# Kernel optimization log

Hardware: AMD Instinct MI355X
Metric: run time of the kernel (lower is better)

Reference implementation:

```python
import jax, jax.numpy as jnp
import numpy as np

N_NODES = 100_000
N_EDGES = 1_600_000
N_GRAPHS = 512
D_NODE = 128
H = 128
L_EXTRA = 2  # model_layer - 1


def _bn(x, g, b, eps=1e-5):
    # BatchNorm1d, training-mode math (biased batch variance), eval dropout = identity
    mu = jnp.mean(x, axis=0)
    var = jnp.var(x, axis=0)
    return g * (x - mu) * jax.lax.rsqrt(var + eps) + b


def _gin_conv(x, src, dst, W1, b1, bng, bnb, W2, b2):
    # GINConv (eps=0): mlp(x + sum_{j->i} x_j); mlp = Lin -> BN -> ReLU -> Lin
    agg = jax.ops.segment_sum(x[src], dst, num_segments=x.shape[0])
    h = x + agg
    h = jax.nn.relu(_bn(h @ W1 + b1, bng, bnb))
    return h @ W2 + b2


def setup_inputs():
    key = jax.random.key(0)
    ks = jax.random.split(key, 24)
    s = 0.05
    d = {}
    d["x"] = jax.random.normal(ks[0], (N_NODES, D_NODE), dtype=jnp.float32)
    d["edge_index"] = jax.random.randint(ks[1], (2, N_EDGES), 0, N_NODES, dtype=jnp.int32)
    d["batch"] = jnp.sort(jax.random.randint(ks[2], (N_NODES,), 0, N_GRAPHS, dtype=jnp.int32))
    d["vn_emb"] = jax.random.normal(ks[3], (1, H)) * s
    # conv1 MLP: Linear(D_NODE, 2H) -> BN -> ReLU -> Linear(2H, H)
    d["c1_W1"] = jax.random.normal(ks[4], (D_NODE, 2 * H)) * s
    d["c1_b1"] = jnp.zeros((2 * H,))
    d["c1_bng"] = jnp.ones((2 * H,))
    d["c1_bnb"] = jnp.zeros((2 * H,))
    d["c1_W2"] = jax.random.normal(ks[5], (2 * H, H)) * s
    d["c1_b2"] = jnp.zeros((H,))
    d["bn1_g"] = jnp.ones((H,))
    d["bn1_b"] = jnp.zeros((H,))
    # stacked extra GIN layers (model_layer - 1)
    d["cW1"] = jax.random.normal(ks[6], (L_EXTRA, H, 2 * H)) * s
    d["cb1"] = jnp.zeros((L_EXTRA, 2 * H))
    d["cbng"] = jnp.ones((L_EXTRA, 2 * H))
    d["cbnb"] = jnp.zeros((L_EXTRA, 2 * H))
    d["cW2"] = jax.random.normal(ks[7], (L_EXTRA, 2 * H, H)) * s
    d["cb2"] = jnp.zeros((L_EXTRA, H))
    d["bns_g"] = jnp.ones((L_EXTRA, H))
    d["bns_b"] = jnp.zeros((L_EXTRA, H))
    # virtual node MLP: Lin(H,2H)->BN->ReLU->Lin(2H,H)->BN->ReLU->Dropout
    d["vW1"] = jax.random.normal(ks[8], (H, 2 * H)) * s
    d["vb1"] = jnp.zeros((2 * H,))
    d["vbn1_g"] = jnp.ones((2 * H,))
    d["vbn1_b"] = jnp.zeros((2 * H,))
    d["vW2"] = jax.random.normal(ks[9], (2 * H, H)) * s
    d["vb2"] = jnp.zeros((H,))
    d["vbn2_g"] = jnp.ones((H,))
    d["vbn2_b"] = jnp.zeros((H,))
    return d


def reference(x, edge_index, batch, vn_emb, c1_W1, c1_b1, c1_bng, c1_bnb, c1_W2, c1_b2,
              bn1_g, bn1_b, cW1, cb1, cbng, cbnb, cW2, cb2, bns_g, bns_b,
              vW1, vb1, vbn1_g, vbn1_b, vW2, vb2, vbn2_g, vbn2_b):
    src, dst = edge_index[0], edge_index[1]
    # virtual node feature per graph: Embedding(1, H) indexed with zeros
    vfeat = jnp.broadcast_to(vn_emb[0], (N_GRAPHS, H))
    # layer 1: dropout is identity in eval mode
    post = jax.nn.relu(_bn(_gin_conv(x, src, dst, c1_W1, c1_b1, c1_bng, c1_bnb, c1_W2, c1_b2), bn1_g, bn1_b))
    for i in range(L_EXTRA):
        post = post + vfeat[batch]                       # virtual-node broadcast
        post = _bn(_gin_conv(post, src, dst, cW1[i], cb1[i], cbng[i], cbnb[i], cW2[i], cb2[i]), bns_g[i], bns_b[i])
        if i < L_EXTRA - 1:
            post = jax.nn.relu(post)
            pooled = jax.ops.segment_sum(post, batch, num_segments=N_GRAPHS)  # GlobalAddPool
            z = pooled + vfeat
            z = jax.nn.relu(_bn(z @ vW1 + vb1, vbn1_g, vbn1_b))
            vfeat = jax.nn.relu(_bn(z @ vW2 + vb2, vbn2_g, vbn2_b))
    # readout: global mean pool over nodes per graph
    counts = jax.ops.segment_sum(jnp.ones((x.shape[0],), post.dtype), batch, num_segments=N_GRAPHS)
    out = jax.ops.segment_sum(post, batch, num_segments=N_GRAPHS) / jnp.maximum(counts, 1.0)[:, None]
    return out
```

## Files before the change

kernel.cpp:

```cpp
#include <hip/hip_runtime.h>

#define NN 100000
#define NE 1600000
#define NG 512
#define DH 128
#define DH2 256
#define SCB 98
#define NSTRIPE 32

typedef __attribute__((ext_vector_type(8))) _Float16 h8;
typedef __attribute__((ext_vector_type(2))) _Float16 h2;
typedef __attribute__((ext_vector_type(4))) float f4;

static inline size_t align256(size_t x) { return (x + 255) & ~size_t(255); }

__global__ __launch_bounds__(256) void countslot_k(const int* __restrict__ ei,
                                                   int* __restrict__ cursor,
                                                   int* __restrict__ slot) {
    int i = blockIdx.x * blockDim.x + threadIdx.x;
    int stride = gridDim.x * blockDim.x;
    for (int e = i; e < NE; e += stride)
        slot[e] = atomicAdd(&cursor[ei[NE + e]], 1);
}

__global__ __launch_bounds__(256) void place_k(const int* __restrict__ ei,
                                               const int* __restrict__ rowptr,
                                               const int* __restrict__ slot,
                                               int* __restrict__ esrc) {
    int i = blockIdx.x * blockDim.x + threadIdx.x;
    int stride = gridDim.x * blockDim.x;
    for (int e = i; e < NE; e += stride)
        esrc[rowptr[ei[NE + e]] + slot[e]] = ei[e];
}

__global__ __launch_bounds__(256) void scan1_k(const int* __restrict__ deg,
                                               int* __restrict__ part) {
    int i0 = blockIdx.x * 1024 + threadIdx.x * 4;
    int s = 0;
    if (i0 < NN) {
        int4 v = *(const int4*)(deg + i0);
        s = v.x + v.y + v.z + v.w;
    }
#pragma unroll
    for (int o = 1; o < 64; o <<= 1) s += __shfl_xor(s, o);
    __shared__ int ws[4];
    if ((threadIdx.x & 63) == 0) ws[threadIdx.x >> 6] = s;
    __syncthreads();
    if (threadIdx.x == 0) part[blockIdx.x] = ws[0] + ws[1] + ws[2] + ws[3];
}

__global__ void scan2_k(int* __restrict__ part, int* __restrict__ rowptr,
                        const int* __restrict__ batch, int* __restrict__ gcnt) {
    int t = threadIdx.x;
    __shared__ int wtot[2];
    int v = 0, s = 0;
    if (t < 128) {
        v = (t < SCB) ? part[t] : 0;
        s = v;
#pragma unroll
        for (int o = 1; o < 64; o <<= 1) {
            int u = __shfl_up(s, o);
            if ((t & 63) >= o) s += u;
        }
        if ((t & 63) == 63) wtot[t >> 6] = s;
    }
    __syncthreads();
    if (t < 128) {
        if (t >= 64) s += wtot[0];
        if (t < SCB) part[t] = s - v;
        if (t == SCB - 1) rowptr[NN] = s;
    }
    for (int g = t; g < NG; g += 256) {
        int lo = 0, hi = NN;
        while (lo < hi) { int m = (lo + hi) >> 1; if (batch[m] < g) lo = m + 1; else hi = m; }
        int b0 = lo;
        lo = 0; hi = NN;
        int g1 = g + 1;
        while (lo < hi) { int m = (lo + hi) >> 1; if (batch[m] < g1) lo = m + 1; else hi = m; }
        gcnt[g] = lo - b0;
    }
}

__global__ __launch_bounds__(256) void scan3_k(const int* __restrict__ deg,
                                               const int* __restrict__ part,
                                               int* __restrict__ rowptr) {
    int t = threadIdx.x;
    int i0 = blockIdx.x * 1024 + t * 4;
    int4 v = {0, 0, 0, 0};
    if (i0 < NN) v = *(const int4*)(deg + i0);
    int s = v.x + v.y + v.z + v.w;
    __shared__ int sc[256];
    sc[t] = s;
    __syncthreads();
    for (int o = 1; o < 256; o <<= 1) {
        int add = (t >= o) ? sc[t - o] : 0;
        __syncthreads();
        sc[t] += add;
        __syncthreads();
    }
    int excl = (t ? sc[t - 1] : 0) + part[blockIdx.x];
    if (i0 < NN) {
        int4 r;
        r.x = excl;
        r.y = excl + v.x;
        r.z = excl + v.x + v.y;
        r.w = excl + v.x + v.y + v.z;
        *(int4*)(rowptr + i0) = r;
    }
}

__global__ void castx_k(const float* __restrict__ x, _Float16* __restrict__ xh,
                        const float* __restrict__ emb, _Float16* __restrict__ vfeat) {
    int i = blockIdx.x * blockDim.x + threadIdx.x;
    if (i < NG * 16) {
        const float* e = emb + (i & 15) * 8;
        h8 v = {(_Float16)e[0], (_Float16)e[1], (_Float16)e[2], (_Float16)e[3],
                (_Float16)e[4], (_Float16)e[5], (_Float16)e[6], (_Float16)e[7]};
        ((h8*)vfeat)[i] = v;
    }
    if (i >= NN * 16) return;
    const float4* s = (const float4*)x + i * 2;
    float4 p = s[0], q = s[1];
    h8 h = {(_Float16)p.x, (_Float16)p.y, (_Float16)p.z, (_Float16)p.w,
            (_Float16)q.x, (_Float16)q.y, (_Float16)q.z, (_Float16)q.w};
    ((h8*)xh)[i] = h;
}

__global__ void zin_k(const float* __restrict__ pooled, const _Float16* __restrict__ vf,
                      _Float16* __restrict__ zb) {
    int i = blockIdx.x * blockDim.x + threadIdx.x;
    if (i < NG * DH) zb[i] = (_Float16)(pooled[i] + (float)vf[i]);
}

__global__ void addvn_k(_Float16* __restrict__ x, const _Float16* __restrict__ vfeat,
                        const int* __restrict__ batch) {
    int i = blockIdx.x * blockDim.x + threadIdx.x;
    if (i >= NN * 16) return;
    int row = i >> 4;
    int bg = batch[row];
    h8 u = ((h8*)x)[i];
    h8 v = ((const h8*)vfeat)[bg * 16 + (i & 15)];
    h8 o;
#pragma unroll
    for (int e = 0; e < 8; e++) o[e] = (_Float16)((float)u[e] + (float)v[e]);
    ((h8*)x)[i] = o;
}

__global__ void finalout_k(const float* __restrict__ pooled2, const int* __restrict__ gcnt,
                           float* __restrict__ outp) {
    int i = blockIdx.x * blockDim.x + threadIdx.x;
    if (i >= NG * DH) return;
    float cnt = (float)gcnt[i >> 7];
    outp[i] = pooled2[i] / fmaxf(cnt, 1.0f);
}

struct WPack {
    const float* w[8];
    _Float16* wt[8];
    int K[8];
    int N[8];
};
__global__ void wtrans_k(WPack p) {
    int id = blockIdx.z;
    const float* W = p.w[id];
    _Float16* Wt = p.wt[id];
    int K = p.K[id], N = p.N[id];
    int n0 = blockIdx.x * 32, k0 = blockIdx.y * 32;
    if (n0 >= N || k0 >= K) return;
    __shared__ float t[32][33];
    int tx = threadIdx.x & 31, ty = threadIdx.x >> 5;
    for (int i = 0; i < 32; i += 8)
        t[ty + i][tx] = W[(size_t)(k0 + ty + i) * N + n0 + tx];
    __syncthreads();
    for (int i = 0; i < 32; i += 8)
        Wt[(size_t)(n0 + ty + i) * K + k0 + tx] = (_Float16)t[tx][ty + i];
}

__global__ __launch_bounds__(256) void agg_k(const _Float16* __restrict__ xin,
                                             const int* __restrict__ rowptr,
                                             const int* __restrict__ esrc,
                                             _Float16* __restrict__ out) {
    int wave = threadIdx.x >> 6, lane = threadIdx.x & 63;
    int node = blockIdx.x * 4 + wave;
    if (node >= NN) return;
    const h2* xr = (const h2*)xin;
    h2 self = xr[(size_t)node * 64 + lane];
    float a0 = (float)self.x, a1 = (float)self.y;
    int beg = rowptr[node], end = rowptr[node + 1];
    int j = beg;
    for (; j + 7 < end; j += 8) {
        int s0 = esrc[j],     s1 = esrc[j + 1], s2 = esrc[j + 2], s3 = esrc[j + 3];
        int s4 = esrc[j + 4], s5 = esrc[j + 5], s6 = esrc[j + 6], s7 = esrc[j + 7];
        h2 u0 = xr[(size_t)s0 * 64 + lane];
        h2 u1 = xr[(size_t)s1 * 64 + lane];
        h2 u2 = xr[(size_t)s2 * 64 + lane];
        h2 u3 = xr[(size_t)s3 * 64 + lane];
        h2 u4 = xr[(size_t)s4 * 64 + lane];
        h2 u5 = xr[(size_t)s5 * 64 + lane];
        h2 u6 = xr[(size_t)s6 * 64 + lane];
        h2 u7 = xr[(size_t)s7 * 64 + lane];
        a0 += ((float)u0.x + (float)u1.x) + ((float)u2.x + (float)u3.x)
            + ((float)u4.x + (float)u5.x) + ((float)u6.x + (float)u7.x);
        a1 += ((float)u0.y + (float)u1.y) + ((float)u2.y + (float)u3.y)
            + ((float)u4.y + (float)u5.y) + ((float)u6.y + (float)u7.y);
    }
    for (; j < end; j++) {
        h2 u = xr[(size_t)esrc[j] * 64 + lane];
        a0 += (float)u.x; a1 += (float)u.y;
    }
    h2 o; o.x = (_Float16)a0; o.y = (_Float16)a1;
    ((h2*)out)[(size_t)node * 64 + lane] = o;
}

__global__ __launch_bounds__(256, 3) void gemmS_k(
        const _Float16* __restrict__ A, const _Float16* __restrict__ Wt,
        const float* __restrict__ bias,
        float* __restrict__ csum, float* __restrict__ csq, int M) {
    constexpr int K = 128;
    constexpr int LDA = K + 8;
    __shared__ __align__(16) _Float16 As[64 * LDA];
    __shared__ __align__(16) _Float16 Ws[128 * LDA];
    const int tid = threadIdx.x;
    const int lane = tid & 63;
    const int wave = tid >> 6;
    const int wr = wave >> 1;
    const int wc = wave & 1;
    const int lm = lane & 15, lq = lane >> 4;
    const int mB = blockIdx.x * 64;

    const int sr = tid >> 4;
    const int sc = (tid & 15) * 8;
#pragma unroll
    for (int rr = 0; rr < 64; rr += 16) {
        int gr = mB + rr + sr; if (gr >= M) gr = M - 1;
        *(h8*)&As[(rr + sr) * LDA + sc] = *(const h8*)&A[(size_t)gr * K + sc];
    }
#pragma unroll
    for (int rr = 0; rr < 128; rr += 16)
        *(h8*)&Ws[(rr + sr) * LDA + sc] = *(const h8*)&Wt[(size_t)(rr + sr) * K + sc];
    __syncthreads();

    f4 acc[2][8];
#pragma unroll
    for (int i = 0; i < 2; i++)
#pragma unroll
        for (int jj = 0; jj < 8; jj++) acc[i][jj] = (f4){0.f, 0.f, 0.f, 0.f};
#pragma unroll
    for (int ct = 0; ct < 2; ct++) {
        if (ct) {
            __syncthreads();
#pragma unroll
            for (int rr = 0; rr < 128; rr += 16)
                *(h8*)&Ws[(rr + sr) * LDA + sc] =
                    *(const h8*)&Wt[(size_t)(128 + rr + sr) * K + sc];
            __syncthreads();
        }
#pragma unroll
        for (int ks = 0; ks < 4; ks++) {
            h8 af[2], bf[4];
#pragma unroll
            for (int i = 0; i < 2; i++)
                af[i] = *(const h8*)&As[(wr * 32 + i * 16 + lm) * LDA + ks * 32 + lq * 8];
#pragma unroll
            for (int j = 0; j < 4; j++)
                bf[j] = *(const h8*)&Ws[(wc * 64 + j * 16 + lm) * LDA + ks * 32 + lq * 8];
#pragma unroll
            for (int i = 0; i < 2; i++)
#pragma unroll
                for (int j = 0; j < 4; j++)
                    acc[i][ct * 4 + j] =
                        __builtin_amdgcn_mfma_f32_16x16x32_f16(af[i], bf[j], acc[i][ct * 4 + j], 0, 0, 0);
        }
    }

    float bv[8];
#pragma unroll
    for (int jj = 0; jj < 8; jj++) bv[jj] = bias[(jj >> 2) * 128 + wc * 64 + (jj & 3) * 16 + lm];
    float ls[8] = {0, 0, 0, 0, 0, 0, 0, 0}, lsq[8] = {0, 0, 0, 0, 0, 0, 0, 0};
#pragma unroll
    for (int i = 0; i < 2; i++) {
        int row = wr * 32 + i * 16 + lq * 4;
#pragma unroll
        for (int jj = 0; jj < 8; jj++) {
#pragma unroll
            for (int r = 0; r < 4; r++) {
                if (mB + row + r < M) {
                    float v = acc[i][jj][r] + bv[jj];
                    ls[jj] += v; lsq[jj] += v * v;
                }
            }
        }
    }
    const int stripe = blockIdx.x & (NSTRIPE - 1);
#pragma unroll
    for (int jj = 0; jj < 8; jj++) {
        float s = ls[jj], q = lsq[jj];
        s += __shfl_xor(s, 16); s += __shfl_xor(s, 32);
        q += __shfl_xor(q, 16); q += __shfl_xor(q, 32);
        if (lq == 0) {
            int col = (jj >> 2) * 128 + wc * 64 + (jj & 3) * 16 + lm;
            atomicAdd(&csum[stripe * 256 + col], s);
            atomicAdd(&csq[stripe * 256 + col], q);
        }
    }
}

__global__ __launch_bounds__(256, 2) void gemmF_k(
        const _Float16* __restrict__ A,
        const _Float16* __restrict__ Wt1,
        const _Float16* __restrict__ Wt2,
        const float* __restrict__ b1v,
        const float* __restrict__ b2v,
        _Float16* __restrict__ C,
        float* __restrict__ csum, float* __restrict__ csq, int M,
        const float* __restrict__ csumIn, const float* __restrict__ csqIn,
        const float* __restrict__ g, const float* __restrict__ b) {
    constexpr int LDA = 136, LDH = 264;
    __shared__ __align__(16) _Float16 Hx[64 * LDH];
    __shared__ __align__(16) _Float16 Ws[128 * LDA];
    __shared__ float s_sc[256], s_sh[256];
    const int tid = threadIdx.x;
    const int lane = tid & 63;
    const int wave = tid >> 6;
    const int wr = wave >> 1;
    const int wc = wave & 1;
    const int lm = lane & 15, lq = lane >> 4;
    const int mB = blockIdx.x * 64;

    {
        float s = 0.f, q = 0.f;
        for (int st = 0; st < NSTRIPE; st++) {
            s += csumIn[st * 256 + tid];
            q += csqIn[st * 256 + tid];
        }
        float invM = 1.0f / (float)M;
        float mean = s * invM;
        float var = q * invM - mean * mean;
        float scv = g[tid] * rsqrtf(var + 1e-5f);
        s_sc[tid] = scv;
        s_sh[tid] = b[tid] - mean * scv;
    }

    const int sr = tid >> 4;
    const int sc = (tid & 15) * 8;
#pragma unroll
    for (int rr = 0; rr < 64; rr += 16) {
        int gr = mB + rr + sr; if (gr >= M) gr = M - 1;
        *(h8*)&Hx[(rr + sr) * LDA + sc] = *(const h8*)&A[(size_t)gr * 128 + sc];
    }
#pragma unroll
    for (int rr = 0; rr < 128; rr += 16)
        *(h8*)&Ws[(rr + sr) * LDA + sc] = *(const h8*)&Wt1[(size_t)(rr + sr) * 128 + sc];
    __syncthreads();

    f4 acc[2][8];
#pragma unroll
    for (int i = 0; i < 2; i++)
#pragma unroll
        for (int jj = 0; jj < 8; jj++) acc[i][jj] = (f4){0.f, 0.f, 0.f, 0.f};
#pragma unroll
    for (int ct = 0; ct < 2; ct++) {
        if (ct) {
            __syncthreads();
#pragma unroll
            for (int rr = 0; rr < 128; rr += 16)
                *(h8*)&Ws[(rr + sr) * LDA + sc] =
                    *(const h8*)&Wt1[(size_t)(128 + rr + sr) * 128 + sc];
            __syncthreads();
        }
#pragma unroll
        for (int ks = 0; ks < 4; ks++) {
            h8 af[2], bf[4];
#pragma unroll
            for (int i = 0; i < 2; i++)
                af[i] = *(const h8*)&Hx[(wr * 32 + i * 16 + lm) * LDA + ks * 32 + lq * 8];
#pragma unroll
            for (int j = 0; j < 4; j++)
                bf[j] = *(const h8*)&Ws[(wc * 64 + j * 16 + lm) * LDA + ks * 32 + lq * 8];
#pragma unroll
            for (int i = 0; i < 2; i++)
#pragma unroll
                for (int j = 0; j < 4; j++)
                    acc[i][ct * 4 + j] =
                        __builtin_amdgcn_mfma_f32_16x16x32_f16(af[i], bf[j], acc[i][ct * 4 + j], 0, 0, 0);
        }
    }
    __syncthreads();

    {
        float bv1[8];
#pragma unroll
        for (int jj = 0; jj < 8; jj++)
            bv1[jj] = b1v[(jj >> 2) * 128 + wc * 64 + (jj & 3) * 16 + lm];
#pragma unroll
        for (int i = 0; i < 2; i++) {
            int row = wr * 32 + i * 16 + lq * 4;
#pragma unroll
            for (int jj = 0; jj < 8; jj++) {
                int col = (jj >> 2) * 128 + wc * 64 + (jj & 3) * 16 + lm;
                float scv = s_sc[col], shv = s_sh[col];
#pragma unroll
                for (int r = 0; r < 4; r++) {
                    float v = acc[i][jj][r] + bv1[jj];
                    v = fmaxf(v * scv + shv, 0.f);
                    Hx[(row + r) * LDH + col] = (_Float16)v;
                }
            }
        }
    }
#pragma unroll
    for (int rr = 0; rr < 128; rr += 16)
        *(h8*)&Ws[(rr + sr) * LDA + sc] = *(const h8*)&Wt2[(size_t)(rr + sr) * 256 + sc];
    __syncthreads();

    f4 acc2[2][4];
#pragma unroll
    for (int i = 0; i < 2; i++)
#pragma unroll
        for (int j = 0; j < 4; j++) acc2[i][j] = (f4){0.f, 0.f, 0.f, 0.f};
#pragma unroll
    for (int kc = 0; kc < 2; kc++) {
        if (kc) {
            __syncthreads();
#pragma unroll
            for (int rr = 0; rr < 128; rr += 16)
                *(h8*)&Ws[(rr + sr) * LDA + sc] =
                    *(const h8*)&Wt2[(size_t)(rr + sr) * 256 + 128 + sc];
            __syncthreads();
        }
#pragma unroll
        for (int ks = 0; ks < 4; ks++) {
            h8 af[2], bf[4];
#pragma unroll
            for (int i = 0; i < 2; i++)
                af[i] = *(const h8*)&Hx[(wr * 32 + i * 16 + lm) * LDH + kc * 128 + ks * 32 + lq * 8];
#pragma unroll
            for (int j = 0; j < 4; j++)
                bf[j] = *(const h8*)&Ws[(wc * 64 + j * 16 + lm) * LDA + ks * 32 + lq * 8];
#pragma unroll
            for (int i = 0; i < 2; i++)
#pragma unroll
                for (int j = 0; j < 4; j++)
                    acc2[i][j] = __builtin_amdgcn_mfma_f32_16x16x32_f16(af[i], bf[j], acc2[i][j], 0, 0, 0);
        }
    }

    const int n0 = wc * 64;
    float bv2[4];
#pragma unroll
    for (int j = 0; j < 4; j++) bv2[j] = b2v[n0 + j * 16 + lm];
    float ls[4] = {0, 0, 0, 0}, lsq[4] = {0, 0, 0, 0};
    __syncthreads();
    _Float16* Cs = Hx;
#pragma unroll
    for (int i = 0; i < 2; i++) {
        int row = wr * 32 + i * 16 + lq * 4;
        bool rv[4];
#pragma unroll
        for (int r = 0; r < 4; r++) rv[r] = (mB + row + r) < M;
#pragma unroll
        for (int j = 0; j < 4; j++) {
#pragma unroll
            for (int r = 0; r < 4; r++) {
                float v = acc2[i][j][r] + bv2[j];
                Cs[(row + r) * LDA + wc * 64 + j * 16 + lm] = (_Float16)v;
                if (rv[r]) { ls[j] += v; lsq[j] += v * v; }
            }
        }
    }
    const int stripe = blockIdx.x & (NSTRIPE - 1);
#pragma unroll
    for (int j = 0; j < 4; j++) {
        float s = ls[j], q = lsq[j];
        s += __shfl_xor(s, 16); s += __shfl_xor(s, 32);
        q += __shfl_xor(q, 16); q += __shfl_xor(q, 32);
        if (lq == 0) {
            atomicAdd(&csum[stripe * 128 + n0 + j * 16 + lm], s);
            atomicAdd(&csq[stripe * 128 + n0 + j * 16 + lm], q);
        }
    }
    __syncthreads();
    const int trow = tid >> 4;
    const int tcol = (tid & 15) * 8;
#pragma unroll
    for (int p = 0; p < 4; p++) {
        int row = p * 16 + trow;
        int grow = mB + row;
        if (grow < M) {
            h8 v = *(const h8*)&Cs[row * LDA + tcol];
            *(h8*)&C[(size_t)grow * 128 + tcol] = v;
        }
    }
}

__global__ void bnrelu_k(const _Float16* __restrict__ in, _Float16* __restrict__ out,
                         const float* __restrict__ csum, const float* __restrict__ csq,
                         const float* __restrict__ g, const float* __restrict__ b,
                         const _Float16* __restrict__ vfeat, const int* __restrict__ batch,
                         int M) {
    constexpr int PER = 16;
    __shared__ float s_sc[128], s_sh[128];
    if (threadIdx.x < 128) {
        int col = threadIdx.x;
        float s = 0.f, q = 0.f;
        for (int st = 0; st < NSTRIPE; st++) {
            s += csum[st * 128 + col];
            q += csq[st * 128 + col];
        }
        float invM = 1.0f / (float)M;
        float mean = s * invM;
        float var = q * invM - mean * mean;
        float scv = g[col] * rsqrtf(var + 1e-5f);
        s_sc[col] = scv;
        s_sh[col] = b[col] - mean * scv;
    }
    __syncthreads();
    int tid = blockIdx.x * blockDim.x + threadIdx.x;
    int c8 = tid % PER;
    int c0 = c8 * 8;
    float sc[8], sh[8];
#pragma unroll
    for (int e = 0; e < 8; e++) { sc[e] = s_sc[c0 + e]; sh[e] = s_sh[c0 + e]; }
    int total = M * PER;
    int stride = gridDim.x * blockDim.x;
    for (int i = tid; i < total; i += stride) {
        int row = i / PER;
        h8 u = ((const h8*)in)[i];
        h8 w;
        bool vn = (vfeat != nullptr);
        if (vn) w = ((const h8*)vfeat)[batch[row] * PER + c8];
        h8 o;
#pragma unroll
        for (int e = 0; e < 8; e++) {
            float vv = fmaxf((float)u[e] * sc[e] + sh[e], 0.f);
            if (vn) vv += (float)w[e];
            o[e] = (_Float16)vv;
        }
        ((h8*)out)[i] = o;
    }
}

__global__ __launch_bounds__(256) void bnpool_k(
        const _Float16* __restrict__ in, _Float16* __restrict__ out,
        const float* __restrict__ csum, const float* __restrict__ csq,
        const float* __restrict__ g, const float* __restrict__ b,
        const int* __restrict__ batch, float* __restrict__ pooled,
        int M, int relu) {
    __shared__ float s_sc[128], s_sh[128];
    if (threadIdx.x < 128) {
        int col = threadIdx.x;
        float s = 0.f, q = 0.f;
        for (int st = 0; st < NSTRIPE; st++) {
            s += csum[st * 128 + col];
            q += csq[st * 128 + col];
        }
        float invM = 1.0f / (float)M;
        float mean = s * invM;
        float var = q * invM - mean * mean;
        float scv = g[col] * rsqrtf(var + 1e-5f);
        s_sc[col] = scv;
        s_sh[col] = b[col] - mean * scv;
    }
    __syncthreads();
    int t = threadIdx.x;
    int c0 = (t & 63) * 2;
    int r0 = blockIdx.x * 128 + (t >> 6) * 32;
    float sc0 = s_sc[c0], h0 = s_sh[c0];
    float sc1 = s_sc[c0 + 1], h1 = s_sh[c0 + 1];
    int rend = r0 + 32; if (rend > M) rend = M;
    float a0 = 0.f, a1 = 0.f; int cur = -1;
    int r = r0;
    for (; r + 1 < rend; r += 2) {
        h2 ua = ((const h2*)in)[(size_t)r * 64 + (c0 >> 1)];
        h2 ub = ((const h2*)in)[(size_t)(r + 1) * 64 + (c0 >> 1)];
        int bga = batch[r], bgb = batch[r + 1];
        float va0 = (float)ua.x * sc0 + h0, va1 = (float)ua.y * sc1 + h1;
        float vb0 = (float)ub.x * sc0 + h0, vb1 = (float)ub.y * sc1 + h1;
        if (relu) {
            va0 = fmaxf(va0, 0.f); va1 = fmaxf(va1, 0.f);
            vb0 = fmaxf(vb0, 0.f); vb1 = fmaxf(vb1, 0.f);
        }
        if (out) {
            h2 oa; oa.x = (_Float16)va0; oa.y = (_Float16)va1;
            h2 ob; ob.x = (_Float16)vb0; ob.y = (_Float16)vb1;
            ((h2*)out)[(size_t)r * 64 + (c0 >> 1)] = oa;
            ((h2*)out)[(size_t)(r + 1) * 64 + (c0 >> 1)] = ob;
        }
        if (bga != cur) {
            if (cur >= 0) {
                atomicAdd(&pooled[(size_t)cur * DH + c0], a0);
                atomicAdd(&pooled[(size_t)cur * DH + c0 + 1], a1);
            }
            cur = bga; a0 = 0.f; a1 = 0.f;
        }
        a0 += va0; a1 += va1;
        if (bgb != cur) {
            atomicAdd(&pooled[(size_t)cur * DH + c0], a0);
            atomicAdd(&pooled[(size_t)cur * DH + c0 + 1], a1);
            cur = bgb; a0 = 0.f; a1 = 0.f;
        }
        a0 += vb0; a1 += vb1;
    }
    for (; r < rend; r++) {
        h2 u = ((const h2*)in)[(size_t)r * 64 + (c0 >> 1)];
        float v0 = (float)u.x * sc0 + h0;
        float v1 = (float)u.y * sc1 + h1;
        if (relu) { v0 = fmaxf(v0, 0.f); v1 = fmaxf(v1, 0.f); }
        if (out) { h2 o; o.x = (_Float16)v0; o.y = (_Float16)v1; ((h2*)out)[(size_t)r * 64 + (c0 >> 1)] = o; }
        int bg = batch[r];
        if (bg != cur) {
            if (cur >= 0) {
                atomicAdd(&pooled[(size_t)cur * DH + c0], a0);
                atomicAdd(&pooled[(size_t)cur * DH + c0 + 1], a1);
            }
            cur = bg; a0 = 0.f; a1 = 0.f;
        }
        a0 += v0; a1 += v1;
    }
    if (cur >= 0) {
        atomicAdd(&pooled[(size_t)cur * DH + c0], a0);
        atomicAdd(&pooled[(size_t)cur * DH + c0 + 1], a1);
    }
}

extern "C" void kernel_launch(void* const* d_in, const int* in_sizes, int n_in,
                              void* d_out, int out_size, void* d_ws, size_t ws_size,
                              hipStream_t stream) {
    const float* x      = (const float*)d_in[0];
    const int*   ei     = (const int*)d_in[1];
    const int*   batch  = (const int*)d_in[2];
    const float* vn_emb = (const float*)d_in[3];
    const float* c1_W1  = (const float*)d_in[4];
    const float* c1_b1  = (const float*)d_in[5];
    const float* c1_bng = (const float*)d_in[6];
    const float* c1_bnb = (const float*)d_in[7];
    const float* c1_W2  = (const float*)d_in[8];
    const float* c1_b2  = (const float*)d_in[9];
    const float* bn1_g  = (const float*)d_in[10];
    const float* bn1_b  = (const float*)d_in[11];
    const float* cW1    = (const float*)d_in[12];
    const float* cb1    = (const float*)d_in[13];
    const float* cbng   = (const float*)d_in[14];
    const float* cbnb   = (const float*)d_in[15];
    const float* cW2    = (const float*)d_in[16];
    const float* cb2    = (const float*)d_in[17];
    const float* bns_g  = (const float*)d_in[18];
    const float* bns_b  = (const float*)d_in[19];
    const float* vW1    = (const float*)d_in[20];
    const float* vb1    = (const float*)d_in[21];
    const float* vbn1_g = (const float*)d_in[22];
    const float* vbn1_b = (const float*)d_in[23];
    const float* vW2    = (const float*)d_in[24];
    const float* vb2    = (const float*)d_in[25];
    const float* vbn2_g = (const float*)d_in[26];
    const float* vbn2_b = (const float*)d_in[27];
    float* outp = (float*)d_out;
    (void)in_sizes; (void)n_in; (void)out_size; (void)ws_size;

    char* w = (char*)d_ws;
    size_t off = 0;
    auto carve = [&](size_t bytes) -> void* {
        void* p = w + off; off = align256(off + bytes); return p;
    };
    int*   cursor  = (int*)carve((size_t)NN * 4);
    float* pooled  = (float*)carve((size_t)NG * DH * 4);
    float* pooled2 = (float*)carve((size_t)NG * DH * 4);
    float *sA[3], *qA[3], *sB[3], *qB[3], *sV1, *qV1, *sV2, *qV2;
    for (int i = 0; i < 3; i++) {
        sA[i] = (float*)carve((size_t)NSTRIPE * 256 * 4);
        qA[i] = (float*)carve((size_t)NSTRIPE * 256 * 4);
    }
    for (int i = 0; i < 3; i++) {
        sB[i] = (float*)carve((size_t)NSTRIPE * 128 * 4);
        qB[i] = (float*)carve((size_t)NSTRIPE * 128 * 4);
    }
    sV1 = (float*)carve((size_t)NSTRIPE * 256 * 4);
    qV1 = (float*)carve((size_t)NSTRIPE * 256 * 4);
    sV2 = (float*)carve((size_t)NSTRIPE * 128 * 4);
    qV2 = (float*)carve((size_t)NSTRIPE * 128 * 4);
    size_t zbytes = off;
    int*   gcnt    = (int*)carve((size_t)NG * 4);
    int*   rowptr  = (int*)carve((size_t)(NN + 1) * 4);
    int*   slot    = (int*)carve((size_t)NE * 4);
    int*   esrc    = (int*)carve((size_t)NE * 4);
    int*   part    = (int*)carve((size_t)SCB * 4);
    _Float16* vfeat = (_Float16*)carve((size_t)NG * DH * 2);
    _Float16* zin   = (_Float16*)carve((size_t)NG * DH * 2);
    _Float16* vraw  = (_Float16*)carve((size_t)NG * DH * 2);
    _Float16* xh    = (_Float16*)carve((size_t)NN * DH * 2);
    _Float16* hb    = (_Float16*)carve((size_t)NN * DH * 2);
    _Float16* abuf  = (_Float16*)carve((size_t)NN * DH * 2);
    _Float16* Wt[8];
    for (int i = 0; i < 8; i++) Wt[i] = (_Float16*)carve((size_t)DH * DH2 * 2);

    WPack wp;
    wp.w[0] = c1_W1;            wp.K[0] = 128; wp.N[0] = 256;
    wp.w[1] = c1_W2;            wp.K[1] = 256; wp.N[1] = 128;
    wp.w[2] = cW1;              wp.K[2] = 128; wp.N[2] = 256;
    wp.w[3] = cW2;              wp.K[3] = 256; wp.N[3] = 128;
    wp.w[4] = cW1 + 128 * 256;  wp.K[4] = 128; wp.N[4] = 256;
    wp.w[5] = cW2 + 256 * 128;  wp.K[5] = 256; wp.N[5] = 128;
    wp.w[6] = vW1;              wp.K[6] = 128; wp.N[6] = 256;
    wp.w[7] = vW2;              wp.K[7] = 256; wp.N[7] = 128;
    for (int i = 0; i < 8; i++) wp.wt[i] = Wt[i];

    const int GB64 = (NN + 63) / 64;
    const int GB   = (NN + 127) / 128;
    const int GV64 = (NG + 63) / 64;

    hipMemsetAsync(d_ws, 0, zbytes, stream);
    countslot_k<<<782, 256, 0, stream>>>(ei, cursor, slot);
    scan1_k<<<SCB, 256, 0, stream>>>(cursor, part);
    scan2_k<<<1, 256, 0, stream>>>(part, rowptr, batch, gcnt);
    scan3_k<<<SCB, 256, 0, stream>>>(cursor, part, rowptr);
    place_k<<<782, 256, 0, stream>>>(ei, rowptr, slot, esrc);
    wtrans_k<<<dim3(8, 8, 8), 256, 0, stream>>>(wp);
    castx_k<<<(NN * 16 + 255) / 256, 256, 0, stream>>>(x, xh, vn_emb, vfeat);

    agg_k<<<NN / 4, 256, 0, stream>>>(xh, rowptr, esrc, hb);
    gemmS_k<<<GB64, 256, 0, stream>>>(hb, Wt[0], c1_b1, sA[0], qA[0], NN);
    gemmF_k<<<GB64, 256, 0, stream>>>(hb, Wt[0], Wt[1], c1_b1, c1_b2, abuf,
                                      sB[0], qB[0], NN, sA[0], qA[0], c1_bng, c1_bnb);
    bnrelu_k<<<2048, 256, 0, stream>>>(abuf, abuf, sB[0], qB[0], bn1_g, bn1_b,
                                       vfeat, batch, NN);

    agg_k<<<NN / 4, 256, 0, stream>>>(abuf, rowptr, esrc, hb);
    gemmS_k<<<GB64, 256, 0, stream>>>(hb, Wt[2], cb1, sA[1], qA[1], NN);
    gemmF_k<<<GB64, 256, 0, stream>>>(hb, Wt[2], Wt[3], cb1, cb2, abuf,
                                      sB[1], qB[1], NN, sA[1], qA[1], cbng, cbnb);
    bnpool_k<<<GB, 256, 0, stream>>>(abuf, abuf, sB[1], qB[1], bns_g, bns_b,
                                     batch, pooled, NN, 1);

    zin_k<<<(NG * DH + 255) / 256, 256, 0, stream>>>(pooled, vfeat, zin);
    gemmS_k<<<GV64, 256, 0, stream>>>(zin, Wt[6], vb1, sV1, qV1, NG);
    gemmF_k<<<GV64, 256, 0, stream>>>(zin, Wt[6], Wt[7], vb1, vb2, vraw,
                                      sV2, qV2, NG, sV1, qV1, vbn1_g, vbn1_b);
    bnrelu_k<<<32, 256, 0, stream>>>(vraw, vfeat, sV2, qV2, vbn2_g, vbn2_b,
                                     nullptr, nullptr, NG);

    addvn_k<<<(NN * 16 + 255) / 256, 256, 0, stream>>>(abuf, vfeat, batch);
    agg_k<<<NN / 4, 256, 0, stream>>>(abuf, rowptr, esrc, hb);
    gemmS_k<<<GB64, 256, 0, stream>>>(hb, Wt[4], cb1 + 256, sA[2], qA[2], NN);
    gemmF_k<<<GB64, 256, 0, stream>>>(hb, Wt[4], Wt[5], cb1 + 256, cb2 + 128, abuf,
                                      sB[2], qB[2], NN, sA[2], qA[2], cbng + 256, cbnb + 256);
    bnpool_k<<<GB, 256, 0, stream>>>(abuf, nullptr, sB[2], qB[2],
                                     bns_g + 128, bns_b + 128, batch, pooled2, NN, 0);

    finalout_k<<<(NG * DH + 255) / 256, 256, 0, stream>>>(pooled2, gcnt, outp);
}
```

Measured before the change: 708.6 us.

## Fuse degree count, input cast and weight transpose into one launch; drop slot array

Merges the edge degree counting, fp32-to-fp16 input cast and weight transpose kernels into a single launch that dispatches on block index. Degree counting no longer records a per-edge slot, so the 6.4MB slot array is neither written nor read. Placement now uses a second atomic cursor initialised from rowptr, and each thread handles four edges through int4 loads. This cuts launch count and memory traffic in CSR construction. In exchange, edge order within each row becomes nondeterministic, which can change the fp summation order in aggregation.

Result: slower. 816.6 us (+15.2%).

```diff
diff --git a/kernel.cpp b/kernel.cpp
--- a/kernel.cpp
+++ b/kernel.cpp
@@ -7,6 +7,9 @@
 #define DH2 256
 #define SCB 98
 #define NSTRIPE 32
+#define EB4 1563
+#define CB 6250
+#define WB 512
 
 typedef __attribute__((ext_vector_type(8))) _Float16 h8;
 typedef __attribute__((ext_vector_type(2))) _Float16 h2;
@@ -14,23 +17,77 @@
 
 static inline size_t align256(size_t x) { return (x + 255) & ~size_t(255); }
 
-__global__ __launch_bounds__(256) void countslot_k(const int* __restrict__ ei,
-                                                   int* __restrict__ cursor,
-                                                   int* __restrict__ slot) {
-    int i = blockIdx.x * blockDim.x + threadIdx.x;
-    int stride = gridDim.x * blockDim.x;
-    for (int e = i; e < NE; e += stride)
-        slot[e] = atomicAdd(&cursor[ei[NE + e]], 1);
+struct WPack {
+    const float* w[8];
+    _Float16* wt[8];
+    int K[8];
+    int N[8];
+};
+
+__global__ __launch_bounds__(256) void csrcast_k(
+        const int* __restrict__ ei, int* __restrict__ cursor,
+        const float* __restrict__ x, _Float16* __restrict__ xh,
+        const float* __restrict__ emb, _Float16* __restrict__ vfeat,
+        WPack p) {
+    __shared__ float t[32][33];
+    int b = blockIdx.x;
+    if (b < EB4) {
+        int i = b * 256 + threadIdx.x;
+        int e = i * 4;
+        if (e >= NE) return;
+        int4 d = *(const int4*)(ei + NE + e);
+        atomicAdd(&cursor[d.x], 1);
+        atomicAdd(&cursor[d.y], 1);
+        atomicAdd(&cursor[d.z], 1);
+        atomicAdd(&cursor[d.w], 1);
+    } else if (b < EB4 + CB) {
+        int i = (b - EB4) * 256 + threadIdx.x;
+        if (i < NG * 16) {
+            const float* e = emb + (i & 15) * 8;
+            h8 v = {(_Float16)e[0], (_Float16)e[1], (_Float16)e[2], (_Float16)e[3],
+                    (_Float16)e[4], (_Float16)e[5], (_Float16)e[6], (_Float16)e[7]};
+            ((h8*)vfeat)[i] = v;
+        }
+        if (i >= NN * 16) return;
+        const float4* s = (const float4*)x + i * 2;
+        float4 pp = s[0], q = s[1];
+        h8 h = {(_Float16)pp.x, (_Float16)pp.y, (_Float16)pp.z, (_Float16)pp.w,
+                (_Float16)q.x, (_Float16)q.y, (_Float16)q.z, (_Float16)q.w};
+        ((h8*)xh)[i] = h;
+    } else {
+        int idx = b - (EB4 + CB);
+        int id = idx >> 6;
+        int rem = idx & 63;
+        const float* W = p.w[id];
+        _Float16* Wt = p.wt[id];
+        int K = p.K[id], N = p.N[id];
+        int n0 = (rem & 7) * 32, k0 = (rem >> 3) * 32;
+        if (n0 >= N || k0 >= K) return;
+        int tx = threadIdx.x & 31, ty = threadIdx.x >> 5;
+        for (int i = 0; i < 32; i += 8)
+            t[ty + i][tx] = W[(size_t)(k0 + ty + i) * N + n0 + tx];
+        __syncthreads();
+        for (int i = 0; i < 32; i += 8)
+            Wt[(size_t)(n0 + ty + i) * K + k0 + tx] = (_Float16)t[tx][ty + i];
+    }
 }
 
 __global__ __launch_bounds__(256) void place_k(const int* __restrict__ ei,
-                                               const int* __restrict__ rowptr,
-                                               const int* __restrict__ slot,
+                                               int* __restrict__ rowcur,
                                                int* __restrict__ esrc) {
     int i = blockIdx.x * blockDim.x + threadIdx.x;
-    int stride = gridDim.x * blockDim.x;
-    for (int e = i; e < NE; e += stride)
-        esrc[rowptr[ei[NE + e]] + slot[e]] = ei[e];
+    int e = i * 4;
+    if (e >= NE) return;
+    int4 d = *(const int4*)(ei + NE + e);
+    int4 sr = *(const int4*)(ei + e);
+    int p0 = atomicAdd(&rowcur[d.x], 1);
+    int p1 = atomicAdd(&rowcur[d.y], 1);
+    int p2 = atomicAdd(&rowcur[d.z], 1);
+    int p3 = atomicAdd(&rowcur[d.w], 1);
+    esrc[p0] = sr.x;
+    esrc[p1] = sr.y;
+    esrc[p2] = sr.z;
+    esrc[p3] = sr.w;
 }
 
 __global__ __launch_bounds__(256) void scan1_k(const int* __restrict__ deg,
@@ -83,7 +140,8 @@
 
 __global__ __launch_bounds__(256) void scan3_k(const int* __restrict__ deg,
                                                const int* __restrict__ part,
-                                               int* __restrict__ rowptr) {
+                                               int* __restrict__ rowptr,
+                                               int* __restrict__ rowcur) {
     int t = threadIdx.x;
     int i0 = blockIdx.x * 1024 + t * 4;
     int4 v = {0, 0, 0, 0};
@@ -103,27 +161,11 @@
         int4 r;
         r.x = excl;
         r.y = excl + v.x;
-        r.z = excl + v.x + v.y;
-        r.w = excl + v.x + v.y + v.z;
+        r.z = r.y + v.y;
+        r.w = r.z + v.z;
         *(int4*)(rowptr + i0) = r;
-    }
-}
-
-__global__ void castx_k(const float* __restrict__ x, _Float16* __restrict__ xh,
-                        const float* __restrict__ emb, _Float16* __restrict__ vfeat) {
-    int i = blockIdx.x * blockDim.x + threadIdx.x;
-    if (i < NG * 16) {
-        const float* e = emb + (i & 15) * 8;
-        h8 v = {(_Float16)e[0], (_Float16)e[1], (_Float16)e[2], (_Float16)e[3],
-                (_Float16)e[4], (_Float16)e[5], (_Float16)e[6], (_Float16)e[7]};
-        ((h8*)vfeat)[i] = v;
-    }
-    if (i >= NN * 16) return;
-    const float4* s = (const float4*)x + i * 2;
-    float4 p = s[0], q = s[1];
-    h8 h = {(_Float16)p.x, (_Float16)p.y, (_Float16)p.z, (_Float16)p.w,
-            (_Float16)q.x, (_Float16)q.y, (_Float16)q.z, (_Float16)q.w};
-    ((h8*)xh)[i] = h;
+        *(int4*)(rowcur + i0) = r;
+    }
 }
 
 __global__ void zin_k(const float* __restrict__ pooled, const _Float16* __restrict__ vf,
@@ -152,28 +194,6 @@
     if (i >= NG * DH) return;
     float cnt = (float)gcnt[i >> 7];
     outp[i] = pooled2[i] / fmaxf(cnt, 1.0f);
-}
-
-struct WPack {
-    const float* w[8];
-    _Float16* wt[8];
-    int K[8];
-    int N[8];
-};
-__global__ void wtrans_k(WPack p) {
-    int id = blockIdx.z;
-    const float* W = p.w[id];
-    _Float16* Wt = p.wt[id];
-    int K = p.K[id], N = p.N[id];
-    int n0 = blockIdx.x * 32, k0 = blockIdx.y * 32;
-    if (n0 >= N || k0 >= K) return;
-    __shared__ float t[32][33];
-    int tx = threadIdx.x & 31, ty = threadIdx.x >> 5;
-    for (int i = 0; i < 32; i += 8)
-        t[ty + i][tx] = W[(size_t)(k0 + ty + i) * N + n0 + tx];
-    __syncthreads();
-    for (int i = 0; i < 32; i += 8)
-        Wt[(size_t)(n0 + ty + i) * K + k0 + tx] = (_Float16)t[tx][ty + i];
 }
 
 __global__ __launch_bounds__(256) void agg_k(const _Float16* __restrict__ xin,
@@ -681,7 +701,7 @@
     size_t zbytes = off;
     int*   gcnt    = (int*)carve((size_t)NG * 4);
     int*   rowptr  = (int*)carve((size_t)(NN + 1) * 4);
-    int*   slot    = (int*)carve((size_t)NE * 4);
+    int*   rowcur  = (int*)carve((size_t)NN * 4);
     int*   esrc    = (int*)carve((size_t)NE * 4);
     int*   part    = (int*)carve((size_t)SCB * 4);
     _Float16* vfeat = (_Float16*)carve((size_t)NG * DH * 2);
@@ -709,13 +729,11 @@
     const int GV64 = (NG + 63) / 64;
 
     hipMemsetAsync(d_ws, 0, zbytes, stream);
-    countslot_k<<<782, 256, 0, stream>>>(ei, cursor, slot);
+    csrcast_k<<<EB4 + CB + WB, 256, 0, stream>>>(ei, cursor, x, xh, vn_emb, vfeat, wp);
     scan1_k<<<SCB, 256, 0, stream>>>(cursor, part);
     scan2_k<<<1, 256, 0, stream>>>(part, rowptr, batch, gcnt);
-    scan3_k<<<SCB, 256, 0, stream>>>(cursor, part, rowptr);
-    place_k<<<782, 256, 0, stream>>>(ei, rowptr, slot, esrc);
-    wtrans_k<<<dim3(8, 8, 8), 256, 0, stream>>>(wp);
-    castx_k<<<(NN * 16 + 255) / 256, 256, 0, stream>>>(x, xh, vn_emb, vfeat);
+    scan3_k<<<SCB, 256, 0, stream>>>(cursor, part, rowptr, rowcur);
+    place_k<<<EB4, 256, 0, stream>>>(ei, rowcur, esrc);
 
     agg_k<<<NN / 4, 256, 0, stream>>>(xh, rowptr, esrc, hb);
     gemmS_k<<<GB64, 256, 0, stream>>>(hb, Wt[0], c1_b1, sA[0], qA[0], NN);
```
